# Kernel optimization log

Measured on AMD Instinct MI355X. Metric: run time of the kernel, lower is better.

## Reference

```python
import math
import jax, jax.numpy as jnp
import numpy as np

# ---- config (from ModelConfig) ----
HIDDEN = 2880
HEAD_DIM = 64
N_HEADS = 64
N_KV = 8
Q_MULT = N_HEADS // N_KV  # 8
SLIDING_WINDOW = 128      # left context; causal windowed attention
ROPE_BASE = 150000.0
ROPE_SCALE = 32.0
NTK_ALPHA = 1.0
NTK_BETA = 32.0
INIT_CTX = 4096
RMS_EPS = 1e-5
SM_SCALE = 1.0 / math.sqrt(HEAD_DIM)
Q_DIM = N_HEADS * HEAD_DIM   # 4096
KV_DIM = N_KV * HEAD_DIM     # 512
QKV_DIM = Q_DIM + 2 * KV_DIM # 5120
B, T = 1, 2048


def _rope_cos_sin(n_tokens):
    """YaRN-scaled rotary cache, per RotaryEmbedding._compute_concentration_and_inv_freq."""
    d_half = HEAD_DIM // 2
    freq = ROPE_BASE ** (jnp.arange(0, HEAD_DIM, 2, dtype=jnp.float32) / HEAD_DIM)
    concentration = 0.1 * math.log(ROPE_SCALE) + 1.0
    low = d_half * math.log(INIT_CTX / (NTK_BETA * 2 * math.pi)) / math.log(ROPE_BASE)
    high = d_half * math.log(INIT_CTX / (NTK_ALPHA * 2 * math.pi)) / math.log(ROPE_BASE)
    interpolation = 1.0 / (ROPE_SCALE * freq)
    extrapolation = 1.0 / freq
    ramp = (jnp.arange(d_half, dtype=jnp.float32) - low) / (high - low)
    mask = 1.0 - jnp.clip(ramp, 0.0, 1.0)
    inv_freq = interpolation * (1.0 - mask) + extrapolation * mask
    pos = jnp.arange(n_tokens, dtype=jnp.float32)
    angles = pos[:, None] * inv_freq[None, :]  # [t, d/2]
    return jnp.cos(angles) * concentration, jnp.sin(angles) * concentration


def _apply_rope(x, cos, sin):
    """Interleaved RoPE (matches _apply_rotary_emb). x: [b, t, ..., d]."""
    shape = x.shape
    n_mid = x.ndim - 3  # dims between token axis and feature axis
    c = cos.reshape((1, shape[1]) + (1,) * n_mid + (shape[-1] // 2,))
    s = sin.reshape((1, shape[1]) + (1,) * n_mid + (shape[-1] // 2,))
    x1 = x[..., ::2]
    x2 = x[..., 1::2]
    o1 = x1 * c - x2 * s
    o2 = x2 * c + x1 * s
    return jnp.stack((o1, o2), axis=-1).reshape(shape)


def _rmsnorm(x, scale):
    t = x.astype(jnp.float32)
    t = t * jax.lax.rsqrt(jnp.mean(t * t, axis=-1, keepdims=True) + RMS_EPS)
    return (t * scale).astype(x.dtype)


def setup_inputs() -> dict:
    key = jax.random.key(0)
    ks = jax.random.split(key, 7)
    x = jax.random.normal(ks[0], (B, T, HIDDEN), dtype=jnp.float32)
    norm_scale = jnp.ones((HIDDEN,), dtype=jnp.float32)
    w_qkv = jax.random.normal(ks[1], (QKV_DIM, HIDDEN), dtype=jnp.float32) * (HIDDEN ** -0.5)
    b_qkv = jax.random.normal(ks[2], (QKV_DIM,), dtype=jnp.float32) * 0.02
    sinks = jax.random.normal(ks[3], (N_HEADS,), dtype=jnp.float32)
    w_out = jax.random.normal(ks[4], (HIDDEN, Q_DIM), dtype=jnp.float32) * (Q_DIM ** -0.5)
    b_out = jax.random.normal(ks[5], (HIDDEN,), dtype=jnp.float32) * 0.02
    return {"x": x, "norm_scale": norm_scale, "w_qkv": w_qkv, "b_qkv": b_qkv,
            "sinks": sinks, "w_out": w_out, "b_out": b_out}


def reference(x, norm_scale, w_qkv, b_qkv, sinks, w_out, b_out):
    b, t, _ = x.shape
    h = _rmsnorm(x, norm_scale)
    qkv = h @ w_qkv.T + b_qkv  # [b, t, 5120]
    q = qkv[..., :Q_DIM].reshape(b, t, N_KV, Q_MULT, HEAD_DIM)
    k = qkv[..., Q_DIM:Q_DIM + KV_DIM].reshape(b, t, N_KV, HEAD_DIM)
    v = qkv[..., Q_DIM + KV_DIM:].reshape(b, t, N_KV, HEAD_DIM)

    cos, sin = _rope_cos_sin(t)
    q = _apply_rope(q, cos, sin)
    k = _apply_rope(k, cos, sin)

    # sliding-window causal attention with sink logits (sdpa windowed path)
    left_ctx = SLIDING_WINDOW
    window = left_ctx + 1
    kp = jnp.pad(k, ((0, 0), (left_ctx, 0), (0, 0), (0, 0)))
    vp = jnp.pad(v, ((0, 0), (left_ctx, 0), (0, 0), (0, 0)))
    gather_idx = jnp.arange(t)[:, None] + jnp.arange(window)[None, :]  # into padded axis
    kwin = kp[:, gather_idx]  # [b, t, w, n_kv, d]
    vwin = vp[:, gather_idx]

    pos = jnp.arange(t)[:, None] + (jnp.arange(window) - left_ctx)[None, :]
    valid = (pos >= 0) & (pos < t)  # [t, w]

    scores = jnp.einsum('bthqd,btwhd->bthqw', q, kwin).astype(jnp.float32) * SM_SCALE
    scores = jnp.where(valid[None, :, None, None, :], scores, -jnp.inf)

    sink = (sinks * math.log(2.0)).reshape(N_KV, Q_MULT)
    sink = jnp.broadcast_to(sink[None, None, :, :, None], (b, t, N_KV, Q_MULT, 1))
    scores = jnp.concatenate([scores, sink], axis=-1)  # [b, t, h, q, w+1]

    w_attn = jax.nn.softmax(scores, axis=-1)[..., :-1].astype(v.dtype)
    attn = jnp.einsum('bthqw,btwhd->bthqd', w_attn, vwin).reshape(b, t, -1)

    out = attn @ w_out.T + b_out
    return x + out
```

## Files before the change

kernel.cpp:

```cpp
#include <hip/hip_runtime.h>
#include <math.h>

typedef unsigned short u16;
typedef unsigned int   u32;
using f32x4  = __attribute__((ext_vector_type(4))) float;
using bf16x8 = __attribute__((ext_vector_type(8))) __bf16;

#define HIDDEN   2880
#define QKVD     5120
#define QD       4096
#define TTOK     2048
#define NKV      8
#define QMULT    8
#define HD       64
#define NPAD     2944

#define PREP_QKV_BLOCKS  14400
#define PREP_RMS_BLOCKS  2048

static __device__ __forceinline__ float bflo(u32 u){ return __uint_as_float(u << 16); }
static __device__ __forceinline__ float bfhi(u32 u){ return __uint_as_float(u & 0xffff0000u); }
static __device__ __forceinline__ u16 f2bf(float f){
    u32 u = __float_as_uint(f);
    u32 r = (u + 0x7fffu + ((u >> 16) & 1u)) >> 16;
    return (u16)r;
}

static __device__ __forceinline__ void glds16(const void* g, void* l) {
    __builtin_amdgcn_global_load_lds(
        (__attribute__((address_space(1))) void*)g,
        (__attribute__((address_space(3))) void*)l,
        16, 0, 0);
}

#define BAR() asm volatile("s_barrier" ::: "memory")

__global__ __launch_bounds__(256) void prep_kernel(const float* __restrict__ w_qkv,
                                                   u16* __restrict__ wqkv_bf,
                                                   const float* __restrict__ x,
                                                   const float* __restrict__ scale,
                                                   u16* __restrict__ h) {
    const int b = blockIdx.x;
    const int tid = threadIdx.x;
    if (b < PREP_QKV_BLOCKS) {
        int i = b * 256 + tid;
        float4 f = ((const float4*)w_qkv)[i];
        ushort4 o;
        o.x = f2bf(f.x); o.y = f2bf(f.y); o.z = f2bf(f.z); o.w = f2bf(f.w);
        ((ushort4*)wqkv_bf)[i] = o;
    } else {
        const int t = b - PREP_QKV_BLOCKS;
        const float4* xr = (const float4*)(x + (long)t * HIDDEN);
        float4 v[3];
        float ss = 0.f;
        #pragma unroll
        for (int it = 0; it < 3; ++it) {
            int i4 = tid + it * 256;
            if (i4 < 720) {
                v[it] = xr[i4];
                ss += v[it].x*v[it].x + v[it].y*v[it].y + v[it].z*v[it].z + v[it].w*v[it].w;
            }
        }
        #pragma unroll
        for (int off = 32; off > 0; off >>= 1) ss += __shfl_down(ss, off);
        __shared__ float red[4];
        if ((tid & 63) == 0) red[tid >> 6] = ss;
        __syncthreads();
        float tot = red[0] + red[1] + red[2] + red[3];
        float rr = rsqrtf(tot * (1.0f / HIDDEN) + 1e-5f);
        ushort4* hr = (ushort4*)(h + (long)t * HIDDEN);
        #pragma unroll
        for (int it = 0; it < 3; ++it) {
            int i4 = tid + it * 256;
            if (i4 < 720) {
                float4 s4 = ((const float4*)scale)[i4];
                ushort4 o;
                o.x = f2bf(v[it].x * rr * s4.x);
                o.y = f2bf(v[it].y * rr * s4.y);
                o.z = f2bf(v[it].z * rr * s4.z);
                o.w = f2bf(v[it].w * rr * s4.w);
                hr[i4] = o;
            }
        }
    }
}


#define READ_BQ(SET, BASE, NQ) do { \
    SET[0][0] = *(const bf16x8*)((BASE) + (2*(NQ)+0)*2048 + off0); \
    SET[0][1] = *(const bf16x8*)((BASE) + (2*(NQ)+0)*2048 + off1); \
    SET[1][0] = *(const bf16x8*)((BASE) + (2*(NQ)+1)*2048 + off0); \
    SET[1][1] = *(const bf16x8*)((BASE) + (2*(NQ)+1)*2048 + off1); \
} while (0)

#define READ_AQ(BASE) do { \
    _Pragma("unroll") \
    for (int mi_ = 0; mi_ < 4; ++mi_) { \
        aq[mi_][0] = *(const bf16x8*)((BASE) + mi_*2048 + off0); \
        aq[mi_][1] = *(const bf16x8*)((BASE) + mi_*2048 + off1); \
    } \
} while (0)

#define MFMA_N(NQ, SET) do { \
    __builtin_amdgcn_s_setprio(1); \
    _Pragma("unroll") \
    for (int mi_ = 0; mi_ < 4; ++mi_) { \
        _Pragma("unroll") \
        for (int j_ = 0; j_ < 2; ++j_) { \
            acc[mi_][2*(NQ)+j_] = __builtin_amdgcn_mfma_f32_16x16x32_bf16(aq[mi_][0], SET[j_][0], acc[mi_][2*(NQ)+j_], 0, 0, 0); \
            acc[mi_][2*(NQ)+j_] = __builtin_amdgcn_mfma_f32_16x16x32_bf16(aq[mi_][1], SET[j_][1], acc[mi_][2*(NQ)+j_], 0, 0, 0); \
        } \
    } \
    __builtin_amdgcn_s_setprio(0); \
} while (0)

__global__ __launch_bounds__(512, 2) void gemm_bt_8ph(const u16* __restrict__ A,
                                                      const u16* __restrict__ B,
                                                      u16* __restrict__ C0,
                                                      int N, int K, int ksplit,
                                                      int blimit, int colmax,
                                                      int nz_gemm,
                                                      const float* __restrict__ wout_src,
                                                      u16* __restrict__ wout_dst) {
    const int tid  = threadIdx.x;

    if ((int)blockIdx.z >= nz_gemm) {
        const long nb = (long)gridDim.x * gridDim.y;
        long bidx = (long)blockIdx.y * gridDim.x + blockIdx.x;
        long i = bidx * 512 + tid;
        const long tot = (long)NPAD * QD / 4;
        const long stride = nb * 512;
        for (; i < tot; i += stride) {
            long idx = i * 4;
            int row = (int)(idx >> 12);
            int col = (int)(idx & 4095);
            ushort4 o;
            if (row < HIDDEN) {
                float4 f = *(const float4*)(wout_src + (long)row * QD + col);
                o.x = f2bf(f.x); o.y = f2bf(f.y); o.z = f2bf(f.z); o.w = f2bf(f.w);
            } else {
                o.x = 0; o.y = 0; o.z = 0; o.w = 0;
            }
            ((ushort4*)wout_dst)[i] = o;
        }
        return;
    }

    extern __shared__ u16 smem[];
    u16* const smA = smem;
    u16* const smB = smem + 2 * 256 * 64;
    const int lane = tid & 63;
    const int wv   = tid >> 6;
    const int wm2  = wv >> 1;
    const int wn2  = wv & 1;
    const long m0  = (long)blockIdx.y * 256;
    const long n0  = (long)blockIdx.x * 256;
    const int kbase = blockIdx.z * ksplit;
    const int NT   = ksplit >> 6;
    u16* C = C0 + (size_t)blockIdx.z * ((size_t)TTOK * N);

    const int srow = tid >> 3;
    const int sg8  = ((tid & 7) ^ (srow & 7)) << 3;
    const int fr   = lane & 15;
    const int off0 = ((lane >> 4) << 4) ^ ((lane & 7) << 4);
    const int off1 = off0 ^ 64;
    const char* aR = (const char*)smA + (wm2 * 64  + fr) * 128;
    const char* bR = (const char*)smB + (wn2 * 128 + fr) * 128;

    f32x4 acc[4][8];
    #pragma unroll
    for (int i = 0; i < 4; ++i)
        #pragma unroll
        for (int j = 0; j < 8; ++j) acc[i][j] = f32x4{0.f, 0.f, 0.f, 0.f};

    const u16* Asrc = A + (m0 + srow) * (long)K + kbase + sg8;
    auto stageA = [&](int t) {
        char* dst = (char*)smA + (t & 1) * 32768 + wv * 1024;
        const u16* src = Asrc + t * 64;
        #pragma unroll
        for (int hj = 0; hj < 4; ++hj)
            glds16(src + (size_t)(hj * 64) * K, dst + hj * 8192);
    };
    auto stageBh = [&](int t, int h) {
        char* dst = (char*)smB + (t & 1) * 32768 + (h * 128 + wv * 8) * 128;
        #pragma unroll
        for (int j = 0; j < 2; ++j) {
            long r = n0 + h * 128 + j * 64 + srow;
            if (r > blimit) r = blimit;
            glds16(B + (size_t)r * K + kbase + t * 64 + sg8, dst + j * 8192);
        }
    };

    bf16x8 aq[4][2], bqE[2][2], bqO[2][2];

    stageA(0);
    stageBh(0, 0); stageBh(0, 1);
    if (NT > 1) {
        stageA(1);
        asm volatile("s_waitcnt vmcnt(4)" ::: "memory");
        stageBh(1, 0);
    } else {
        asm volatile("s_waitcnt vmcnt(0)" ::: "memory");
    }
    BAR();
    READ_BQ(bqE, bR, 0);
    READ_AQ(aR);
    BAR();

    for (int t = 0; t < NT; ++t) {
        const char* aS1 = aR + ((t + 1) & 1) * 32768;
        const char* bS  = bR + (t & 1) * 32768;
        const char* bS1 = bR + ((t + 1) & 1) * 32768;
        READ_BQ(bqO, bS, 1);
        if (t + 1 < NT) stageBh(t + 1, 1);
        if (t + 2 < NT) stageA(t + 2);
        BAR();
        MFMA_N(0, bqE);
        BAR();
        READ_BQ(bqE, bS, 2);
        BAR();
        MFMA_N(1, bqO);
        BAR();
        READ_BQ(bqO, bS, 3);
        BAR();
        MFMA_N(2, bqE);
        BAR();
        if (t + 2 < NT)      asm volatile("s_waitcnt vmcnt(4)" ::: "memory");
        else if (t + 1 < NT) asm volatile("s_waitcnt vmcnt(0)" ::: "memory");
        if (t + 2 < NT) stageBh(t + 2, 0);
        BAR();
        MFMA_N(3, bqO);
        if (t + 1 < NT) {
            READ_BQ(bqE, bS1, 0);
            READ_AQ(aS1);
        }
        BAR();
    }

    const int cr = (lane >> 4) * 4;
    const int cc = lane & 15;
    #pragma unroll
    for (int nf = 0; nf < 8; ++nf) {
        long col = n0 + wn2 * 128 + nf * 16 + cc;
        if (col < colmax) {
            #pragma unroll
            for (int mi = 0; mi < 4; ++mi) {
                long row = m0 + wm2 * 64 + mi * 16 + cr;
                #pragma unroll
                for (int r2 = 0; r2 < 4; ++r2)
                    C[(row + r2) * (long)N + col] = f2bf(acc[mi][nf][r2]);
            }
        }
    }
}

__global__ __launch_bounds__(256) void rope_kernel(const u16* __restrict__ p1,
                                                   const float* __restrict__ b_qkv,
                                                   u16* __restrict__ qr,
                                                   u16* __restrict__ kr,
                                                   u16* __restrict__ vr) {
    const int t = blockIdx.x;
    const int tid = threadIdx.x;
    __shared__ float cs[32], sn[32];
    if (tid < 32) {
        float fi = (float)tid;
        float freq   = exp2f(17.1946032f * (fi * (1.0f / 32.0f)));
        float interp = 1.0f / (32.0f * freq);
        float extra  = 1.0f / freq;
        float ramp   = (fi - 8.0927802f) * (1.0f / (17.3980220f - 8.0927802f));
        float rc     = fminf(fmaxf(ramp, 0.0f), 1.0f);
        float invf   = interp * rc + extra * (1.0f - rc);
        float ang    = (float)t * invf;
        cs[tid] = cosf(ang) * 1.3465736f;
        sn[tid] = sinf(ang) * 1.3465736f;
    }
    __syncthreads();
    const u16* rowA = p1 + (long)t * QKVD;
    auto pair = [&](int col) -> float2 {
        u32 ua = *(const u32*)(rowA + col);
        float2 bb = *(const float2*)(b_qkv + col);
        return make_float2(bflo(ua) + bb.x, bfhi(ua) + bb.y);
    };
    for (int p = tid; p < 2048; p += 256) {
        int hd2 = p >> 5, i = p & 31;
        float2 ab = pair(hd2 * 64 + 2 * i);
        float o1 = ab.x * cs[i] - ab.y * sn[i];
        float o2 = ab.y * cs[i] + ab.x * sn[i];
        *(u32*)(qr + (long)t * QD + hd2 * 64 + 2 * i) = (u32)f2bf(o1) | ((u32)f2bf(o2) << 16);
    }
    {
        int kv = tid >> 5, i = tid & 31;
        float2 ab = pair(QD + kv * 64 + 2 * i);
        float o1 = ab.x * cs[i] - ab.y * sn[i];
        float o2 = ab.y * cs[i] + ab.x * sn[i];
        *(u32*)(kr + ((long)kv * TTOK + t) * HD + 2 * i) = (u32)f2bf(o1) | ((u32)f2bf(o2) << 16);
    }
    {
        int kv = tid >> 5, d2 = tid & 31;
        float2 ab = pair(QD + 512 + kv * 64 + 2 * d2);
        *(u32*)(vr + ((long)kv * TTOK + t) * HD + 2 * d2) = (u32)f2bf(ab.x) | ((u32)f2bf(ab.y) << 16);
    }
}

__global__ __launch_bounds__(256, 2) void attn_kernel(const u16* __restrict__ qr,
                                                      const u16* __restrict__ kr,
                                                      const u16* __restrict__ vr,
                                                      const float* __restrict__ sinks,
                                                      u16* __restrict__ o) {
    const int t0  = blockIdx.x * 16;
    const int h   = blockIdx.y;
    const int qhg = blockIdx.z;
    const int tid = threadIdx.x;
    const int lane = tid & 63, wv = tid >> 6;
    __shared__ __align__(16) u16 ks[144][72];
    __shared__ __align__(16) u16 Vt[64][168];
    __shared__ __align__(16) u16 P [4][16][168];
    const u16* kb = kr + (long)h * TTOK * HD;
    const u16* vb = vr + (long)h * TTOK * HD;

    #pragma unroll
    for (int i = 0; i < 5; ++i) {
        int idx = i * 256 + tid;
        if (idx < 144 * 8) {
            int rr = idx >> 3, c = idx & 7;
            int tk = t0 - 128 + rr;
            int tks = tk < 0 ? 0 : tk;
            *(uint4*)&ks[rr][c * 8] = *(const uint4*)(kb + (long)tks * HD + c * 8);
        }
    }
    #pragma unroll
    for (int c4 = 0; c4 < 8; ++c4) {
        if (tid < 144) {
            int tk = t0 - 128 + tid;
            int tks = tk < 0 ? 0 : tk;
            uint4 v4 = *(const uint4*)(vb + (long)tks * HD + c4 * 8);
            int d0 = c4 * 8;
            Vt[d0+0][tid] = (u16)(v4.x & 0xffff); Vt[d0+1][tid] = (u16)(v4.x >> 16);
            Vt[d0+2][tid] = (u16)(v4.y & 0xffff); Vt[d0+3][tid] = (u16)(v4.y >> 16);
            Vt[d0+4][tid] = (u16)(v4.z & 0xffff); Vt[d0+5][tid] = (u16)(v4.z >> 16);
            Vt[d0+6][tid] = (u16)(v4.w & 0xffff); Vt[d0+7][tid] = (u16)(v4.w >> 16);
        }
    }
    if (tid < 128) {
        *(uint4*)&Vt[tid >> 1][144 + (tid & 1) * 8] = uint4{0, 0, 0, 0};
    }
    if (lane < 32) {
        *(uint4*)&P[wv][lane >> 1][144 + (lane & 1) * 8] = uint4{0, 0, 0, 0};
    }
    __syncthreads();

    const int qh   = qhg * 4 + wv;
    const int head = h * QMULT + qh;
    const int fr = lane & 15, fk = (lane >> 4) * 8;
    const int cr = (lane >> 4) * 4;

    const u16* qrow = qr + (long)(t0 + fr) * QD + head * HD;
    bf16x8 qf0 = *(const bf16x8*)(qrow + fk);
    bf16x8 qf1 = *(const bf16x8*)(qrow + 32 + fk);

    const int kmin = 128 - t0;
    float lsum[4] = {0.f, 0.f, 0.f, 0.f};

    for (int nt = 0; nt < 9; ++nt) {
        bf16x8 b0 = *(const bf16x8*)&ks[nt * 16 + fr][fk];
        bf16x8 b1 = *(const bf16x8*)&ks[nt * 16 + fr][32 + fk];
        f32x4 s = f32x4{0.f, 0.f, 0.f, 0.f};
        s = __builtin_amdgcn_mfma_f32_16x16x32_bf16(qf0, b0, s, 0, 0, 0);
        s = __builtin_amdgcn_mfma_f32_16x16x32_bf16(qf1, b1, s, 0, 0, 0);
        const int kk = nt * 16 + fr;
        #pragma unroll
        for (int r = 0; r < 4; ++r) {
            int row = cr + r;
            bool valid = (kk >= row) && (kk <= row + 128) && (kk >= kmin);
            float p = valid ? __expf(s[r] * 0.125f) : 0.0f;
            lsum[r] += p;
            P[wv][row][kk] = f2bf(p);
        }
    }

    f32x4 oacc[4];
    #pragma unroll
    for (int dt = 0; dt < 4; ++dt) oacc[dt] = f32x4{0.f, 0.f, 0.f, 0.f};
    #pragma unroll
    for (int k5 = 0; k5 < 5; ++k5) {
        const int k0 = k5 * 32;
        bf16x8 pa = *(const bf16x8*)&P[wv][fr][k0 + fk];
        #pragma unroll
        for (int dt = 0; dt < 4; ++dt) {
            bf16x8 vf = *(const bf16x8*)&Vt[dt * 16 + fr][k0 + fk];
            oacc[dt] = __builtin_amdgcn_mfma_f32_16x16x32_bf16(pa, vf, oacc[dt], 0, 0, 0);
        }
    }

    #pragma unroll
    for (int r = 0; r < 4; ++r) {
        float v = lsum[r];
        v += __shfl_xor(v, 1);
        v += __shfl_xor(v, 2);
        v += __shfl_xor(v, 4);
        v += __shfl_xor(v, 8);
        lsum[r] = v;
    }
    const float sk = exp2f(sinks[head]);
    float inv[4];
    #pragma unroll
    for (int r = 0; r < 4; ++r) inv[r] = 1.0f / (lsum[r] + sk);

    #pragma unroll
    for (int dt = 0; dt < 4; ++dt) {
        #pragma unroll
        for (int r = 0; r < 4; ++r) {
            o[(long)(t0 + cr + r) * QD + head * HD + dt * 16 + fr] = f2bf(oacc[dt][r] * inv[r]);
        }
    }
}

__global__ __launch_bounds__(256) void reduce2_kernel(const u16* __restrict__ p2a,
                                                      const u16* __restrict__ p2b,
                                                      const float* __restrict__ x,
                                                      const float* __restrict__ b_out,
                                                      float* __restrict__ out) {
    const int row = blockIdx.y;
    const int c4 = blockIdx.x * 256 + threadIdx.x;
    if (c4 >= 720) return;
    const int col = c4 * 4;
    ushort4 ua = *(const ushort4*)(p2a + (long)row * NPAD + col);
    ushort4 ub = *(const ushort4*)(p2b + (long)row * NPAD + col);
    float4 xv = *(const float4*)(x + (long)row * HIDDEN + col);
    float4 bv = *(const float4*)(b_out + col);
    float4 o;
    o.x = xv.x + bv.x + __uint_as_float((u32)ua.x << 16) + __uint_as_float((u32)ub.x << 16);
    o.y = xv.y + bv.y + __uint_as_float((u32)ua.y << 16) + __uint_as_float((u32)ub.y << 16);
    o.z = xv.z + bv.z + __uint_as_float((u32)ua.z << 16) + __uint_as_float((u32)ub.z << 16);
    o.w = xv.w + bv.w + __uint_as_float((u32)ua.w << 16) + __uint_as_float((u32)ub.w << 16);
    *(float4*)(out + (long)row * HIDDEN + col) = o;
}

extern "C" void kernel_launch(void* const* d_in, const int* in_sizes, int n_in,
                              void* d_out, int out_size, void* d_ws, size_t ws_size,
                              hipStream_t stream) {
    const float* x      = (const float*)d_in[0];
    const float* nscale = (const float*)d_in[1];
    const float* w_qkv  = (const float*)d_in[2];
    const float* b_qkv  = (const float*)d_in[3];
    const float* sinks  = (const float*)d_in[4];
    const float* w_out  = (const float*)d_in[5];
    const float* b_out  = (const float*)d_in[6];
    float* out = (float*)d_out;

    static int smem_set = 0;
    if (!smem_set) {
        hipFuncSetAttribute((const void*)gemm_bt_8ph,
                            hipFuncAttributeMaxDynamicSharedMemorySize, 131072);
        smem_set = 1;
    }

    char* ws = (char*)d_ws;
    size_t off = 0;
    auto alloc = [&](size_t bytes) { void* p = ws + off; off += (bytes + 255) & ~(size_t)255; return p; };
    u16* wqkv_bf = (u16*)alloc((size_t)QKVD * HIDDEN * 2);
    u16* wout_bf = (u16*)alloc((size_t)NPAD * QD * 2);
    u16* h       = (u16*)alloc((size_t)TTOK * HIDDEN * 2);
    u16* p1      = (u16*)alloc((size_t)2 * TTOK * QKVD * 2);
    u16* qrot    = (u16*)alloc((size_t)TTOK * QD * 2);
    u16* krot    = (u16*)alloc((size_t)NKV * TTOK * HD * 2);
    u16* vrot    = (u16*)alloc((size_t)NKV * TTOK * HD * 2);
    u16* attn = wqkv_bf;
    u16* p2   = p1;

    prep_kernel<<<PREP_QKV_BLOCKS + PREP_RMS_BLOCKS, 256, 0, stream>>>(
        w_qkv, wqkv_bf, x, nscale, h);
    gemm_bt_8ph<<<dim3(QKVD / 256, TTOK / 256, 2), 512, 131072, stream>>>(
        h, wqkv_bf, p1, QKVD, HIDDEN, HIDDEN, QKVD - 1, QKVD, 1, w_out, wout_bf);
    rope_kernel<<<TTOK, 256, 0, stream>>>(p1, b_qkv, qrot, krot, vrot);
    attn_kernel<<<dim3(TTOK / 16, NKV, 2), 256, 0, stream>>>(qrot, krot, vrot, sinks, attn);
    gemm_bt_8ph<<<dim3((NPAD + 255) / 256, TTOK / 256, 2), 512, 131072, stream>>>(
        attn, wout_bf, p2, NPAD, QD, QD / 2, NPAD - 1, NPAD, 2, nullptr, nullptr);
    reduce2_kernel<<<dim3(3, TTOK), 256, 0, stream>>>(
        p2, p2 + (size_t)TTOK * NPAD, x, b_out, out);
}
```

Baseline: 337.5 us.

## Split QKV GEMM K dimension into up to three slabs and trim GEMM barriers

```diff
diff --git a/kernel.cpp b/kernel.cpp
--- a/kernel.cpp
+++ b/kernel.cpp
@@ -156,7 +156,8 @@
     const long m0  = (long)blockIdx.y * 256;
     const long n0  = (long)blockIdx.x * 256;
     const int kbase = blockIdx.z * ksplit;
-    const int NT   = ksplit >> 6;
+    int krem = K - kbase; if (krem > ksplit) krem = ksplit;
+    const int NT   = krem >> 6;
     u16* C = C0 + (size_t)blockIdx.z * ((size_t)TTOK * N);
 
     const int srow = tid >> 3;
@@ -197,8 +198,8 @@
     stageBh(0, 0); stageBh(0, 1);
     if (NT > 1) {
         stageA(1);
-        asm volatile("s_waitcnt vmcnt(4)" ::: "memory");
         stageBh(1, 0);
+        asm volatile("s_waitcnt vmcnt(6)" ::: "memory");
     } else {
         asm volatile("s_waitcnt vmcnt(0)" ::: "memory");
     }
@@ -214,26 +215,20 @@
         READ_BQ(bqO, bS, 1);
         if (t + 1 < NT) stageBh(t + 1, 1);
         if (t + 2 < NT) stageA(t + 2);
-        BAR();
         MFMA_N(0, bqE);
         BAR();
         READ_BQ(bqE, bS, 2);
-        BAR();
         MFMA_N(1, bqO);
         BAR();
         READ_BQ(bqO, bS, 3);
-        BAR();
         MFMA_N(2, bqE);
-        BAR();
         if (t + 2 < NT)      asm volatile("s_waitcnt vmcnt(4)" ::: "memory");
         else if (t + 1 < NT) asm volatile("s_waitcnt vmcnt(0)" ::: "memory");
+        BAR();
+        if (t + 1 < NT) READ_BQ(bqE, bS1, 0);
         if (t + 2 < NT) stageBh(t + 2, 0);
-        BAR();
         MFMA_N(3, bqO);
-        if (t + 1 < NT) {
-            READ_BQ(bqE, bS1, 0);
-            READ_AQ(aS1);
-        }
+        if (t + 1 < NT) READ_AQ(aS1);
         BAR();
     }
 
@@ -258,7 +253,8 @@
                                                    const float* __restrict__ b_qkv,
                                                    u16* __restrict__ qr,
                                                    u16* __restrict__ kr,
-                                                   u16* __restrict__ vr) {
+                                                   u16* __restrict__ vr,
+                                                   int nsplit) {
     const int t = blockIdx.x;
     const int tid = threadIdx.x;
     __shared__ float cs[32], sn[32];
@@ -277,9 +273,13 @@
     __syncthreads();
     const u16* rowA = p1 + (long)t * QKVD;
     auto pair = [&](int col) -> float2 {
-        u32 ua = *(const u32*)(rowA + col);
         float2 bb = *(const float2*)(b_qkv + col);
-        return make_float2(bflo(ua) + bb.x, bfhi(ua) + bb.y);
+        float a = bb.x, b = bb.y;
+        for (int s = 0; s < nsplit; ++s) {
+            u32 u = *(const u32*)(rowA + (size_t)s * TTOK * QKVD + col);
+            a += bflo(u); b += bfhi(u);
+        }
+        return make_float2(a, b);
     };
     for (int p = tid; p < 2048; p += 256) {
         int hd2 = p >> 5, i = p & 31;
@@ -455,24 +455,33 @@
         smem_set = 1;
     }
 
+    const size_t slab = (size_t)TTOK * QKVD * 2;
+    const size_t fixed = ((size_t)QKVD * HIDDEN * 2)
+                       + ((size_t)NPAD * QD * 2)
+                       + ((size_t)TTOK * HIDDEN * 2)
+                       + ((size_t)TTOK * QD * 2)
+                       + 4096;
+    const int gs1 = (fixed + 3 * slab <= ws_size) ? 3 : 2;
+
     char* ws = (char*)d_ws;
     size_t off = 0;
     auto alloc = [&](size_t bytes) { void* p = ws + off; off += (bytes + 255) & ~(size_t)255; return p; };
     u16* wqkv_bf = (u16*)alloc((size_t)QKVD * HIDDEN * 2);
     u16* wout_bf = (u16*)alloc((size_t)NPAD * QD * 2);
     u16* h       = (u16*)alloc((size_t)TTOK * HIDDEN * 2);
-    u16* p1      = (u16*)alloc((size_t)2 * TTOK * QKVD * 2);
+    u16* p1      = (u16*)alloc((size_t)gs1 * slab);
     u16* qrot    = (u16*)alloc((size_t)TTOK * QD * 2);
-    u16* krot    = (u16*)alloc((size_t)NKV * TTOK * HD * 2);
-    u16* vrot    = (u16*)alloc((size_t)NKV * TTOK * HD * 2);
     u16* attn = wqkv_bf;
+    u16* krot = wqkv_bf + (size_t)TTOK * QD;
+    u16* vrot = krot + (size_t)NKV * TTOK * HD;
     u16* p2   = p1;
 
     prep_kernel<<<PREP_QKV_BLOCKS + PREP_RMS_BLOCKS, 256, 0, stream>>>(
         w_qkv, wqkv_bf, x, nscale, h);
-    gemm_bt_8ph<<<dim3(QKVD / 256, TTOK / 256, 2), 512, 131072, stream>>>(
-        h, wqkv_bf, p1, QKVD, HIDDEN, HIDDEN, QKVD - 1, QKVD, 1, w_out, wout_bf);
-    rope_kernel<<<TTOK, 256, 0, stream>>>(p1, b_qkv, qrot, krot, vrot);
+    const int ks1 = (gs1 == 3) ? (HIDDEN / 3) : 1472;
+    gemm_bt_8ph<<<dim3(QKVD / 256, TTOK / 256, gs1 + 1), 512, 131072, stream>>>(
+        h, wqkv_bf, p1, QKVD, HIDDEN, ks1, QKVD - 1, QKVD, gs1, w_out, wout_bf);
+    rope_kernel<<<TTOK, 256, 0, stream>>>(p1, b_qkv, qrot, krot, vrot, gs1);
     attn_kernel<<<dim3(TTOK / 16, NKV, 2), 256, 0, stream>>>(qrot, krot, vrot, sinks, attn);
     gemm_bt_8ph<<<dim3((NPAD + 255) / 256, TTOK / 256, 2), 512, 131072, stream>>>(
         attn, wout_bf, p2, NPAD, QD, QD / 2, NPAD - 1, NPAD, 2, nullptr, nullptr);
```

Result: slower. 355.9 us (+5.5%).
